# Kernel tuning notes

Hardware: AMD Instinct MI355X
Metric: run time of the kernel (lower is better)

The kernel has to match this reference:

```python
import jax, jax.numpy as jnp
import numpy as np

DIM = 4096; H = 32; D = 128; EPS = 1e-5
BLOCK = 16
BD = 8; MAXB = 64                    # decode seqs, blocks per decode seq
PB = 2; PSEQ = 1024; TP = PB * PSEQ  # prefill: 2 seqs x 1024 tokens
TOK = TP + BD
NBLOCKS = BD * MAXB + TP // BLOCK    # 640
NEG = -1e30


def setup_inputs() -> dict:
    key = jax.random.key(0)
    ks = jax.random.split(key, 10)
    std = 0.02
    x = jax.random.normal(ks[0], (TOK, DIM), jnp.float32)
    key_heap = jax.random.normal(ks[1], (NBLOCKS, BLOCK, H, D), jnp.float32)
    val_heap = jax.random.normal(ks[2], (NBLOCKS, BLOCK, H, D), jnp.float32)
    # decode seq i owns blocks [i*MAXB, (i+1)*MAXB); context_len includes the new token
    ctx = jax.random.randint(ks[3], (BD,), 256, MAXB * BLOCK + 1).astype(jnp.int32)
    block_table = (jnp.arange(BD)[:, None] * MAXB + jnp.arange(MAXB)[None, :]).astype(jnp.int32)
    prefill_slots = BD * MAXB * BLOCK + jnp.arange(TP)      # prefill fills blocks after decode region
    decode_slots = jnp.arange(BD) * MAXB * BLOCK + (ctx - 1)  # newest-token slot per decode seq
    slot_mapping = jnp.concatenate([prefill_slots, decode_slots]).astype(jnp.int32)
    cu = (jnp.arange(PB + 1) * PSEQ).astype(jnp.int32)
    return dict(
        x=x, key_heap=key_heap, val_heap=val_heap,
        slot_mapping=slot_mapping, decode_block_table=block_table,
        decode_context_lens=ctx, prefill_cu_seqlens=cu,
        num_prefill_tokens=TP, prefill_max_seqlen=PSEQ, decode_max_seq_len=MAXB * BLOCK,
        norm1_w=1.0 + std * jax.random.normal(ks[4], (DIM,), jnp.float32),
        norm2_w=1.0 + std * jax.random.normal(ks[5], (DIM,), jnp.float32),
        w_qkv_w=std * jax.random.normal(ks[6], (3 * H * D, DIM), jnp.float32),
        wo_w=std * jax.random.normal(ks[7], (DIM, H * D), jnp.float32),
        w_gate_up_w=std * jax.random.normal(ks[8], (8 * DIM, DIM), jnp.float32),
        w2_w=std * jax.random.normal(ks[9], (DIM, 4 * DIM), jnp.float32),
    )


def _rmsnorm(x, w):
    return x * jax.lax.rsqrt(jnp.mean(x * x, -1, keepdims=True) + EPS) * w


def _forward(x, key_heap, val_heap, norm1_w, norm2_w, w_qkv_w, wo_w, w_gate_up_w, w2_w,
             slot_mapping, decode_block_table, decode_context_lens, prefill_cu_seqlens,
             num_prefill_tokens):
    T = x.shape[0]
    scale = 1.0 / np.sqrt(D)
    residual = x
    # fused norm1 -> QKV projection
    qkv = (_rmsnorm(x, norm1_w) @ w_qkv_w.T).reshape(T, 3, H, D)
    q, k, v = qkv[:, 0], qkv[:, 1], qkv[:, 2]
    # paged cache write (ops.reshape_and_cache)
    nb, bs = key_heap.shape[0], key_heap.shape[1]
    key_flat = key_heap.reshape(nb * bs, H, D).at[slot_mapping].set(k)
    val_flat = val_heap.reshape(nb * bs, H, D).at[slot_mapping].set(v)
    # prefill: varlen causal self-attention (flash_attn_varlen_func)
    Tp = num_prefill_tokens
    pos = jnp.arange(Tp)
    seg = jnp.searchsorted(prefill_cu_seqlens, pos, side='right') - 1
    mask = (seg[:, None] == seg[None, :]) & (pos[:, None] >= pos[None, :])  # [Tp,Tp]
    s = jnp.einsum('ihd,jhd->hij', q[:Tp], k[:Tp]) * scale
    attn_p = jnp.einsum('hij,jhd->ihd',
                        jax.nn.softmax(jnp.where(mask[None], s, NEG), -1), v[:Tp])
    # decode: paged attention over cached KV (ops.paged_attention_v2)
    kd = key_flat.reshape(nb, bs, H, D)[decode_block_table].reshape(BD, -1, H, D)
    vd = val_flat.reshape(nb, bs, H, D)[decode_block_table].reshape(BD, -1, H, D)
    L = kd.shape[1]
    sd = jnp.einsum('bhd,blhd->bhl', q[Tp:], kd) * scale
    dmask = jnp.arange(L)[None, :] < decode_context_lens[:, None]
    attn_d = jnp.einsum('bhl,blhd->bhd',
                        jax.nn.softmax(jnp.where(dmask[:, None, :], sd, NEG), -1), vd)
    attn = jnp.concatenate([attn_p.reshape(Tp, H * D), attn_d.reshape(BD, H * D)], 0)
    # MLP: wo + residual, norm2, SwiGLU, down-proj, residual
    h = attn @ wo_w.T + residual
    residual = h
    gu = _rmsnorm(h, norm2_w) @ w_gate_up_w.T
    g, u = jnp.split(gu, 2, -1)
    return (jax.nn.silu(g) * u) @ w2_w.T + residual


def reference(x, key_heap, val_heap, slot_mapping, decode_block_table, decode_context_lens,
              prefill_cu_seqlens, num_prefill_tokens, prefill_max_seqlen, decode_max_seq_len,
              norm1_w, norm2_w, w_qkv_w, wo_w, w_gate_up_w, w2_w):
    del prefill_max_seqlen, decode_max_seq_len  # kernel scheduling hints only
    return _forward(x, key_heap, val_heap, norm1_w, norm2_w, w_qkv_w, wo_w, w_gate_up_w, w2_w,
                    slot_mapping, decode_block_table, decode_context_lens, prefill_cu_seqlens,
                    num_prefill_tokens)
```

## Files before the change

kernel.cpp:

```cpp
#include <hip/hip_runtime.h>
#include <hip/hip_bf16.h>
#include <stdint.h>

#define DIMC   4096
#define HC     32
#define DC     128
#define TPC    2048
#define TOKC   2056
#define BDC    8
#define MAXBC  64
#define PSEQC  1024
#define QKVN   12288
#define FFNC   16384
#define PSCALE 0.08838834764831843f

typedef __attribute__((ext_vector_type(8))) short short8;
typedef __attribute__((ext_vector_type(4))) float f32x4;
typedef __attribute__((ext_vector_type(4))) unsigned short u16x4;
typedef __attribute__((ext_vector_type(8))) unsigned short u16x8;

__device__ inline unsigned short f2bf(float f) {
  union { float f; unsigned u; } v; v.f = f;
  unsigned r = v.u + 0x7FFFu + ((v.u >> 16) & 1u);
  return (unsigned short)(r >> 16);
}
__device__ inline float bf2f(unsigned short u) {
  union { unsigned u; float f; } v; v.u = ((unsigned)u) << 16;
  return v.f;
}
__device__ inline f32x4 mfma16(short8 a, short8 b, f32x4 c) {
  return __builtin_amdgcn_mfma_f32_16x16x32_bf16(a, b, c, 0, 0, 0);
}
__device__ inline void gload16(const void* g, void* l) {
  __builtin_amdgcn_global_load_lds(
      (const __attribute__((address_space(1))) void*)g,
      (__attribute__((address_space(3))) void*)l, 16, 0, 0);
}

__global__ __launch_bounds__(256) void cvt_w(
    const float* __restrict__ in, unsigned short* __restrict__ out, long n8)
{
  long i = (long)blockIdx.x * 256 + threadIdx.x;
  const long stride = (long)gridDim.x * 256;
  for (; i < n8; i += stride) {
    f32x4 a = ((const f32x4*)in)[2 * i];
    f32x4 b = ((const f32x4*)in)[2 * i + 1];
    u16x8 o;
#pragma unroll
    for (int j = 0; j < 4; ++j) { o[j] = f2bf(a[j]); o[j + 4] = f2bf(b[j]); }
    ((u16x8*)out)[i] = o;
  }
}

__global__ __launch_bounds__(256) void rmsnorm_k(
    const float* __restrict__ x, const float* __restrict__ w,
    unsigned short* __restrict__ out)
{
  const int row = blockIdx.x;
  const int tid = threadIdx.x;
  const f32x4* xr = (const f32x4*)(x + (size_t)row * DIMC);
  f32x4 v[4];
  float ss = 0.f;
#pragma unroll
  for (int i = 0; i < 4; ++i) {
    v[i] = xr[i * 256 + tid];
    ss += v[i][0]*v[i][0] + v[i][1]*v[i][1] + v[i][2]*v[i][2] + v[i][3]*v[i][3];
  }
  for (int off = 32; off; off >>= 1) ss += __shfl_xor(ss, off);
  __shared__ float sred[4];
  if ((tid & 63) == 0) sred[tid >> 6] = ss;
  __syncthreads();
  const float rms = rsqrtf((sred[0]+sred[1]+sred[2]+sred[3]) * (1.f/DIMC) + 1e-5f);
  const f32x4* wr = (const f32x4*)w;
#pragma unroll
  for (int i = 0; i < 4; ++i) {
    f32x4 wv = wr[i * 256 + tid];
    u16x4 o;
#pragma unroll
    for (int j = 0; j < 4; ++j) o[j] = f2bf(v[i][j] * rms * wv[j]);
    *(u16x4*)(out + (size_t)row * DIMC + (size_t)(i * 256 + tid) * 4) = o;
  }
}

template<int MODE>
__global__ __launch_bounds__(512, 2) void gemm8p(
    const unsigned short* __restrict__ A, const unsigned short* __restrict__ Bh,
    float* __restrict__ Cf, unsigned short* __restrict__ Cb,
    const float* __restrict__ Res, int M, int N, int K)
{
  __shared__ char ldsc[131072];
  const int tid = threadIdx.x;
  const int lane = tid & 63, wid = tid >> 6;
  const int wr = wid >> 2, wc = wid & 3;
  const int lhi = lane >> 4, llo = lane & 15;

  const int nM = (M + 255) >> 8;
  const int nwg = gridDim.x, orig = blockIdx.x;
  const int qq = nwg >> 3, rr = nwg & 7;
  const int xcd = orig & 7, lid = orig >> 3;
  const int wgid = (xcd < rr ? xcd*(qq+1) : rr*(qq+1) + (xcd-rr)*qq) + lid;
  const int bm = (wgid % nM) << 8;
  const int bn = (wgid / nM) << 8;

  const unsigned short* src[2][2][2];
#pragma unroll
  for (int i = 0; i < 2; ++i) {
    int s = i * 512 + tid;
    int row = s >> 3;
    int chunk = (s & 7) ^ (row & 7);
#pragma unroll
    for (int h = 0; h < 2; ++h) {
      int ga = bm + h * 128 + row; ga = ga < M ? ga : M - 1;
      src[0][h][i] = A  + (size_t)ga * K + chunk * 8;
      src[1][h][i] = Bh + (size_t)(bn + h * 128 + row) * K + chunk * 8;
    }
  }
  const int NT = K >> 6;

#define STG(U, OP, H) do { \
    int bb_ = (((U) & 1) << 16) + ((OP) << 15) + ((H) << 14) + (wid << 10); \
    gload16(src[OP][H][0] + ((size_t)(U) << 6), ldsc + bb_); \
    gload16(src[OP][H][1] + ((size_t)(U) << 6), ldsc + bb_ + 8192); \
  } while (0)

#define LDA(PB, HA) do { _Pragma("unroll") for (int m_ = 0; m_ < 4; ++m_) { \
    int row_ = wr*64 + m_*16 + llo; \
    int rb_ = (PB) + ((HA) << 14) + row_*128; int sx_ = (row_ & 7) << 4; \
    ar[m_][0] = *(const short8*)(ldsc + rb_ + ((lhi*16) ^ sx_)); \
    ar[m_][1] = *(const short8*)(ldsc + rb_ + ((64 + lhi*16) ^ sx_)); } } while (0)

#define LDB(PB, HB, DST) do { _Pragma("unroll") for (int n_ = 0; n_ < 2; ++n_) { \
    int row_ = wc*32 + n_*16 + llo; \
    int rb_ = (PB) + 32768 + ((HB) << 14) + row_*128; int sx_ = (row_ & 7) << 4; \
    DST[n_][0] = *(const short8*)(ldsc + rb_ + ((lhi*16) ^ sx_)); \
    DST[n_][1] = *(const short8*)(ldsc + rb_ + ((64 + lhi*16) ^ sx_)); } } while (0)

#define MM(QA, QB, B_) do { __builtin_amdgcn_s_setprio(1); \
    _Pragma("unroll") for (int m_ = 0; m_ < 4; ++m_) \
    _Pragma("unroll") for (int n_ = 0; n_ < 2; ++n_) { \
      acc[QA][QB][m_][n_] = mfma16(ar[m_][0], B_[n_][0], acc[QA][QB][m_][n_]); \
      acc[QA][QB][m_][n_] = mfma16(ar[m_][1], B_[n_][1], acc[QA][QB][m_][n_]); } \
    __builtin_amdgcn_s_setprio(0); } while (0)

#define WAITL do { asm volatile("s_waitcnt lgkmcnt(0)" ::: "memory"); \
    __builtin_amdgcn_sched_barrier(0); } while (0)
#define BAR __builtin_amdgcn_s_barrier()

  f32x4 acc[2][2][4][2] = {};
  short8 ar[4][2], b0[2][2], b1[2][2];

  STG(0, 0, 0); STG(0, 0, 1); STG(0, 1, 0); STG(0, 1, 1);
  STG(1, 0, 0); STG(1, 1, 0); STG(1, 1, 1);
  asm volatile("s_waitcnt vmcnt(6)" ::: "memory");
  BAR;

  for (int t = 0; t < NT; ++t) {
    const int pb = (t & 1) << 16;
    LDA(pb, 0); LDB(pb, 0, b0);
    if (t + 1 < NT) STG(t + 1, 0, 1);
    BAR; WAITL;
    MM(0, 0, b0);
    BAR;
    LDB(pb, 1, b1);
    if (t + 2 < NT) STG(t + 2, 0, 0);
    BAR; WAITL;
    MM(0, 1, b1);
    BAR;
    LDA(pb, 1);
    if (t + 2 < NT) STG(t + 2, 1, 0);
    BAR; WAITL;
    MM(1, 1, b1);
    BAR;
    if (t + 2 < NT) {
      STG(t + 2, 1, 1);
      asm volatile("s_waitcnt vmcnt(6)" ::: "memory");
    } else {
      asm volatile("s_waitcnt vmcnt(0)" ::: "memory");
    }
    BAR;
    __builtin_amdgcn_sched_barrier(0);
    MM(1, 0, b0);
    BAR;
  }

#pragma unroll
  for (int qa = 0; qa < 2; ++qa)
#pragma unroll
  for (int m_ = 0; m_ < 4; ++m_)
#pragma unroll
  for (int j = 0; j < 4; ++j) {
    int row = bm + qa*128 + wr*64 + m_*16 + lhi*4 + j;
    if (row < M) {
#pragma unroll
      for (int qb = 0; qb < 2; ++qb)
#pragma unroll
      for (int n_ = 0; n_ < 2; ++n_) {
        int col = bn + qb*128 + wc*32 + n_*16 + llo;
        float v = acc[qa][qb][m_][n_][j];
        if (MODE == 1) { v += Res[(size_t)row*N + col]; Cf[(size_t)row*N + col] = v; }
        else Cb[(size_t)row*N + col] = f2bf(v);
      }
    }
  }
#undef STG
#undef LDA
#undef LDB
#undef MM
#undef WAITL
#undef BAR
}

template<int MODE, int BF16B>
__global__ __launch_bounds__(256) void gemm_bt(
    const unsigned short* __restrict__ A, const float* __restrict__ Bf,
    const unsigned short* __restrict__ Bh,
    float* __restrict__ Cf, unsigned short* __restrict__ Cb,
    const float* __restrict__ Res, int M, int N, int K)
{
  __shared__ unsigned short la[128 * 64];
  __shared__ unsigned short lb[128 * 64];
  const int tid = threadIdx.x;
  const int lane = tid & 63, wid = tid >> 6;
  const int wr = wid >> 1, wc = wid & 1;
  const int lhi = lane >> 4, llo = lane & 15;

  const int nM = (M + 127) >> 7;
  const int nwg = gridDim.x;
  const int orig = blockIdx.x;
  const int qq = nwg >> 3, rr = nwg & 7;
  const int xcd = orig & 7, lid = orig >> 3;
  const int wgid = (xcd < rr ? xcd * (qq + 1) : rr * (qq + 1) + (xcd - rr) * qq) + lid;
  const int bm = (wgid % nM) * 128;
  const int bn = (wgid / nM) * 128;

  const unsigned short* aSrc[4];
  const unsigned short* bSrcH[4];
  char* aDst[4];
  char* bDst[4];
#pragma unroll
  for (int p = 0; p < 4; ++p) {
    int slot = p * 256 + tid;
    int row = slot >> 3;
    int chunk = (slot & 7) ^ (row & 7);
    int gr = bm + row; gr = gr < M ? gr : M - 1;
    aSrc[p] = A + (size_t)gr * K + chunk * 8;
    aDst[p] = (char*)la + p * 4096 + wid * 1024;
    if (BF16B) {
      bSrcH[p] = Bh + (size_t)(bn + row) * K + chunk * 8;
      bDst[p] = (char*)lb + p * 4096 + wid * 1024;
    }
  }

  f32x4 acc[4][4] = {};

  for (int k0 = 0; k0 < K; k0 += 64) {
#pragma unroll
    for (int p = 0; p < 4; ++p) gload16(aSrc[p] + k0, aDst[p]);
    if (BF16B) {
#pragma unroll
      for (int p = 0; p < 4; ++p) gload16(bSrcH[p] + k0, bDst[p]);
    } else {
#pragma unroll
      for (int p = 0; p < 4; ++p) {
        int idx = p * 256 + tid;
        int row = idx >> 3, c8 = (idx & 7) << 3;
        const float* srcf = Bf + (size_t)(bn + row) * K + k0 + c8;
        f32x4 v0 = *(const f32x4*)srcf;
        f32x4 v1 = *(const f32x4*)(srcf + 4);
        short8 bv;
#pragma unroll
        for (int i = 0; i < 4; ++i) { bv[i] = (short)f2bf(v0[i]); bv[i+4] = (short)f2bf(v1[i]); }
        int byt = (row << 7) + (c8 << 1);
        byt ^= (row & 7) << 4;
        *(short8*)((char*)lb + byt) = bv;
      }
    }
    __syncthreads();
#pragma unroll
    for (int kk = 0; kk < 64; kk += 32) {
      short8 af[4], bfr[4];
#pragma unroll
      for (int m = 0; m < 4; ++m) {
        int row = wr * 64 + m * 16 + llo;
        int byt = (row << 7) + ((kk + lhi * 8) << 1);
        byt ^= (row & 7) << 4;
        af[m] = *(const short8*)((const char*)la + byt);
      }
#pragma unroll
      for (int n = 0; n < 4; ++n) {
        int row = wc * 64 + n * 16 + llo;
        int byt = (row << 7) + ((kk + lhi * 8) << 1);
        byt ^= (row & 7) << 4;
        bfr[n] = *(const short8*)((const char*)lb + byt);
      }
#pragma unroll
      for (int m = 0; m < 4; ++m)
#pragma unroll
        for (int n = 0; n < 4; ++n)
          acc[m][n] = mfma16(af[m], bfr[n], acc[m][n]);
    }
    __syncthreads();
  }

#pragma unroll
  for (int m = 0; m < 4; ++m) {
#pragma unroll
    for (int j = 0; j < 4; ++j) {
      int row = bm + wr * 64 + m * 16 + lhi * 4 + j;
      if (row < M) {
#pragma unroll
        for (int n = 0; n < 4; ++n) {
          int col = bn + wc * 64 + n * 16 + llo;
          float v = acc[m][n][j];
          if (MODE == 1) {
            v += Res[(size_t)row * N + col];
            Cf[(size_t)row * N + col] = v;
          } else {
            Cb[(size_t)row * N + col] = f2bf(v);
          }
        }
      }
    }
  }
}

__global__ __launch_bounds__(256) void prefill_attn(
    const unsigned short* __restrict__ qkv, unsigned short* __restrict__ attnb)
{
  const int h = blockIdx.x, qt = blockIdx.y, s = blockIdx.z;
  const int seq0 = s * PSEQC;
  const int q0 = qt * 64;
  const int tid = threadIdx.x;
  const int lane = tid & 63, w = tid >> 6;
  const int lhi = lane >> 4, llo = lane & 15;

  __shared__ unsigned short lk[64 * 128];
  __shared__ unsigned short lvt[128 * 72];
  __shared__ unsigned short lp[4][16 * 72];

  short8 qf[4];
  {
    const unsigned short* qrow =
        qkv + (size_t)(seq0 + q0 + w * 16 + llo) * QKVN + h * DC;
#pragma unroll
    for (int kk = 0; kk < 4; ++kk)
      qf[kk] = *(const short8*)(qrow + kk * 32 + lhi * 8);
  }

  float m_r[4], l_r[4];
#pragma unroll
  for (int r = 0; r < 4; ++r) { m_r[r] = -1e30f; l_r[r] = 0.f; }
  f32x4 oacc[8] = {};

  const int ntiles = qt + 1;
  for (int t = 0; t < ntiles; ++t) {
    const int j0 = t * 64;
#pragma unroll
    for (int p = 0; p < 4; ++p) {
      int idx = p * 256 + tid;
      int row = idx >> 4, c8 = (idx & 15) << 3;
      short8 kv = *(const short8*)(qkv + (size_t)(seq0 + j0 + row) * QKVN + DIMC + h * DC + c8);
      *(short8*)(lk + row * 128 + (c8 ^ ((row & 7) << 3))) = kv;
    }
#pragma unroll
    for (int p = 0; p < 4; ++p) {
      int idx = p * 256 + tid;
      int j = idx >> 4, c8 = (idx & 15) << 3;
      short8 vv = *(const short8*)(qkv + (size_t)(seq0 + j0 + j) * QKVN + 2 * DIMC + h * DC + c8);
#pragma unroll
      for (int i = 0; i < 8; ++i) {
        int d = c8 + i;
        int jj = j ^ (((d >> 3) & 7) << 3);
        lvt[d * 72 + jj] = (unsigned short)vv[i];
      }
    }
    __syncthreads();

    f32x4 sfr[4] = {};
#pragma unroll
    for (int n = 0; n < 4; ++n) {
      int row = n * 16 + llo;
#pragma unroll
      for (int kk = 0; kk < 4; ++kk) {
        int col = (kk * 32 + lhi * 8) ^ ((row & 7) << 3);
        short8 kf = *(const short8*)(lk + row * 128 + col);
        sfr[n] = mfma16(qf[kk], kf, sfr[n]);
      }
    }

    const bool diag = (t == ntiles - 1);
    const int qbase = q0 + w * 16 + lhi * 4;
    float pv[4][4];
#pragma unroll
    for (int r = 0; r < 4; ++r) {
      float mx = -1e30f;
#pragma unroll
      for (int n = 0; n < 4; ++n) {
        float sv = sfr[n][r] * PSCALE;
        if (diag && (j0 + n * 16 + llo > qbase + r)) sv = -1e30f;
        pv[n][r] = sv;
        mx = fmaxf(mx, sv);
      }
      for (int off = 8; off; off >>= 1) mx = fmaxf(mx, __shfl_xor(mx, off));
      float mnew = fmaxf(m_r[r], mx);
      float alpha = __expf(m_r[r] - mnew);
      m_r[r] = mnew;
      float rs = 0.f;
#pragma unroll
      for (int n = 0; n < 4; ++n) {
        float p = __expf(pv[n][r] - mnew);
        pv[n][r] = p;
        rs += p;
      }
      for (int off = 8; off; off >>= 1) rs += __shfl_xor(rs, off);
      l_r[r] = l_r[r] * alpha + rs;
#pragma unroll
      for (int f = 0; f < 8; ++f) oacc[f][r] *= alpha;
    }

    unsigned short* lpw = lp[w];
#pragma unroll
    for (int r = 0; r < 4; ++r)
#pragma unroll
      for (int n = 0; n < 4; ++n)
        lpw[(lhi * 4 + r) * 72 + n * 16 + llo] = f2bf(pv[n][r]);

#pragma unroll
    for (int kk = 0; kk < 2; ++kk) {
      short8 pf = *(const short8*)(lpw + llo * 72 + kk * 32 + lhi * 8);
#pragma unroll
      for (int f = 0; f < 8; ++f) {
        int d = f * 16 + llo;
        int jb = kk * 32 + lhi * 8;
        int jj = jb ^ (((d >> 3) & 7) << 3);
        short8 vf = *(const short8*)(lvt + d * 72 + jj);
        oacc[f] = mfma16(pf, vf, oacc[f]);
      }
    }
    __syncthreads();
  }

#pragma unroll
  for (int r = 0; r < 4; ++r) {
    int row = seq0 + q0 + w * 16 + lhi * 4 + r;
    float inv = 1.f / l_r[r];
#pragma unroll
    for (int f = 0; f < 8; ++f)
      attnb[(size_t)row * DIMC + h * DC + f * 16 + llo] = f2bf(oacc[f][r] * inv);
  }
}

__global__ __launch_bounds__(256) void decode_attn(
    const unsigned short* __restrict__ qkv,
    const float* __restrict__ kheap, const float* __restrict__ vheap,
    const int* __restrict__ btab, const int* __restrict__ ctxl,
    unsigned short* __restrict__ attnb)
{
  const int h = blockIdx.x, b = blockIdx.y;
  const int ctx = ctxl[b];
  const int tq = TPC + b;
  const int tid = threadIdx.x;
  __shared__ float sq[DC];
  __shared__ float sp[1024];
  __shared__ float sred[4];
  __shared__ float obuf[DC];

  const unsigned short* qrow = qkv + (size_t)tq * QKVN + h * DC;
  if (tid < DC) sq[tid] = bf2f(qrow[tid]);
  __syncthreads();

  float lmax = -1e30f;
#pragma unroll
  for (int i = 0; i < 4; ++i) {
    int l = i * 256 + tid;
    float sv = -1e30f;
    if (l < ctx) {
      float accd = 0.f;
      if (l == ctx - 1) {
        const unsigned short* kn = qkv + (size_t)tq * QKVN + DIMC + h * DC;
        for (int d = 0; d < DC; ++d) accd += sq[d] * bf2f(kn[d]);
      } else {
        int blk = btab[b * MAXBC + (l >> 4)];
        const float* kp = kheap + (((size_t)blk * 16 + (l & 15)) * HC + h) * DC;
#pragma unroll
        for (int d = 0; d < DC; d += 4) {
          f32x4 kv = *(const f32x4*)(kp + d);
          accd += sq[d] * kv[0] + sq[d+1] * kv[1] + sq[d+2] * kv[2] + sq[d+3] * kv[3];
        }
      }
      sv = accd * PSCALE;
    }
    sp[l] = sv;
    lmax = fmaxf(lmax, sv);
  }
  for (int off = 32; off; off >>= 1) lmax = fmaxf(lmax, __shfl_xor(lmax, off));
  if ((tid & 63) == 0) sred[tid >> 6] = lmax;
  __syncthreads();
  const float m = fmaxf(fmaxf(sred[0], sred[1]), fmaxf(sred[2], sred[3]));
  __syncthreads();

  float lsum = 0.f;
#pragma unroll
  for (int i = 0; i < 4; ++i) {
    int l = i * 256 + tid;
    float p = __expf(sp[l] - m);
    sp[l] = p;
    lsum += p;
  }
  for (int off = 32; off; off >>= 1) lsum += __shfl_xor(lsum, off);
  if ((tid & 63) == 0) sred[tid >> 6] = lsum;
  __syncthreads();
  const float denom = sred[0] + sred[1] + sred[2] + sred[3];

  const int d = tid & 127, half = tid >> 7;
  float o = 0.f;
  for (int l = half; l < ctx; l += 2) {
    float p = sp[l];
    float v;
    if (l == ctx - 1) {
      v = bf2f(qkv[(size_t)tq * QKVN + 2 * DIMC + h * DC + d]);
    } else {
      int blk = btab[b * MAXBC + (l >> 4)];
      v = vheap[(((size_t)blk * 16 + (l & 15)) * HC + h) * DC + d];
    }
    o += p * v;
  }
  if (half) obuf[d] = o;
  __syncthreads();
  if (!half)
    attnb[(size_t)tq * DIMC + h * DC + d] = f2bf((o + obuf[d]) / denom);
}

__global__ __launch_bounds__(256) void silu_mul(
    const unsigned short* __restrict__ gu, unsigned short* __restrict__ act)
{
  size_t chunk = (size_t)blockIdx.x * 256 + threadIdx.x;
  size_t row = chunk >> 11;
  int c = (int)(chunk & 2047) << 3;
  const unsigned short* g = gu + row * (2 * FFNC) + c;
  u16x8 gv = *(const u16x8*)g;
  u16x8 uv = *(const u16x8*)(g + FFNC);
  u16x8 o;
#pragma unroll
  for (int i = 0; i < 8; ++i) {
    float gf = bf2f(gv[i]);
    float uf = bf2f(uv[i]);
    float sf = gf / (1.f + __expf(-gf));
    o[i] = f2bf(sf * uf);
  }
  *(u16x8*)(act + row * FFNC + c) = o;
}

extern "C" void kernel_launch(void* const* d_in, const int* in_sizes, int n_in,
                              void* d_out, int out_size, void* d_ws, size_t ws_size,
                              hipStream_t stream) {
  const float* x     = (const float*)d_in[0];
  const float* kheap = (const float*)d_in[1];
  const float* vheap = (const float*)d_in[2];
  const int*   btab  = (const int*)d_in[4];
  const int*   ctxl  = (const int*)d_in[5];
  const float* n1w   = (const float*)d_in[10];
  const float* n2w   = (const float*)d_in[11];
  const float* wqkv  = (const float*)d_in[12];
  const float* wo    = (const float*)d_in[13];
  const float* wgu   = (const float*)d_in[14];
  const float* w2    = (const float*)d_in[15];
  float* out = (float*)d_out;

  char* ws = (char*)d_ws;
  unsigned short* xn   = (unsigned short*)(ws);
  unsigned short* qkvb = (unsigned short*)(ws + 16842752);
  unsigned short* actb = qkvb;
  unsigned short* attn = (unsigned short*)(ws + 16842752 + 67371008);
  float*          hbuf = (float*)(ws + 16842752 + 67371008 + 16842752);
  unsigned short* gub  = (unsigned short*)(ws + 16842752 + 67371008 + 16842752 + 33685504);

  const size_t wbase = 269484032;
  const bool bw = ws_size >= wbase + 536870912ull;
  unsigned short* wqkv_h = (unsigned short*)(ws + wbase);
  unsigned short* wo_h   = (unsigned short*)(ws + wbase + 100663296);
  unsigned short* wgu_h  = (unsigned short*)(ws + wbase + 100663296 + 33554432);
  unsigned short* w2_h   = (unsigned short*)(ws + wbase + 100663296 + 33554432 + 268435456);

  if (bw) {
    cvt_w<<<2048, 256, 0, stream>>>(wqkv, wqkv_h, (long)QKVN * DIMC / 8);
    cvt_w<<<2048, 256, 0, stream>>>(wo,   wo_h,   (long)DIMC * DIMC / 8);
    cvt_w<<<2048, 256, 0, stream>>>(wgu,  wgu_h,  (long)2 * FFNC * DIMC / 8);
    cvt_w<<<2048, 256, 0, stream>>>(w2,   w2_h,   (long)DIMC * FFNC / 8);
  }

  const int nM8 = 9;
  const int nM4 = 17;

  rmsnorm_k<<<TOKC, 256, 0, stream>>>(x, n1w, xn);
  if (bw) gemm8p<2><<<nM8 * (QKVN/256), 512, 0, stream>>>(xn, wqkv_h, nullptr, qkvb, nullptr, TOKC, QKVN, DIMC);
  else    gemm_bt<2,0><<<nM4 * (QKVN/128), 256, 0, stream>>>(xn, wqkv, nullptr, nullptr, qkvb, nullptr, TOKC, QKVN, DIMC);
  prefill_attn<<<dim3(HC, PSEQC / 64, 2), 256, 0, stream>>>(qkvb, attn);
  decode_attn<<<dim3(HC, BDC), 256, 0, stream>>>(qkvb, kheap, vheap, btab, ctxl, attn);
  if (bw) gemm_bt<1,1><<<nM4 * (DIMC/128), 256, 0, stream>>>(attn, nullptr, wo_h, hbuf, nullptr, x, TOKC, DIMC, DIMC);
  else    gemm_bt<1,0><<<nM4 * (DIMC/128), 256, 0, stream>>>(attn, wo, nullptr, hbuf, nullptr, x, TOKC, DIMC, DIMC);
  rmsnorm_k<<<TOKC, 256, 0, stream>>>(hbuf, n2w, xn);
  if (bw) gemm8p<2><<<nM8 * (2*FFNC/256), 512, 0, stream>>>(xn, wgu_h, nullptr, gub, nullptr, TOKC, 2*FFNC, DIMC);
  else    gemm_bt<2,0><<<nM4 * (2*FFNC/128), 256, 0, stream>>>(xn, wgu, nullptr, nullptr, gub, nullptr, TOKC, 2*FFNC, DIMC);
  silu_mul<<<(TOKC * (FFNC / 8)) / 256, 256, 0, stream>>>(gub, actb);
  if (bw) gemm8p<1><<<nM8 * (DIMC/256), 512, 0, stream>>>(actb, w2_h, out, nullptr, hbuf, TOKC, DIMC, FFNC);
  else    gemm_bt<1,0><<<nM4 * (DIMC/128), 256, 0, stream>>>(actb, w2, nullptr, out, nullptr, hbuf, TOKC, DIMC, FFNC);
}
```

Measured before the change: 2.017 ms.

## Add split-K to down-projection GEMM and restructure gemm8p LDS prefetch pipeline

The down-projection GEMM (K=16384, N=4096) only launched 9x16=144 workgroups, which underfills the GPU. It now splits K four ways, writing fp32 partials that a separate reduction kernel sums together with the residual. The shared gemm8p main loop is also rewritten to double-buffer A/B register fragments, prefetching the next tile's LDS reads before the current MFMAs and using vmcnt-gated barriers in place of lgkmcnt waits. The costs are an extra partial buffer of about 135MB plus a reduction pass, and the split-K path is only taken when the workspace is large enough.

```diff
diff --git a/kernel.cpp b/kernel.cpp
--- a/kernel.cpp
+++ b/kernel.cpp
@@ -82,7 +82,7 @@
   }
 }
 
-template<int MODE>
+template<int MODE, int SK>
 __global__ __launch_bounds__(512, 2) void gemm8p(
     const unsigned short* __restrict__ A, const unsigned short* __restrict__ Bh,
     float* __restrict__ Cf, unsigned short* __restrict__ Cb,
@@ -95,12 +95,19 @@
   const int lhi = lane >> 4, llo = lane & 15;
 
   const int nM = (M + 255) >> 8;
+  const int nN = N >> 8;
   const int nwg = gridDim.x, orig = blockIdx.x;
   const int qq = nwg >> 3, rr = nwg & 7;
   const int xcd = orig & 7, lid = orig >> 3;
   const int wgid = (xcd < rr ? xcd*(qq+1) : rr*(qq+1) + (xcd-rr)*qq) + lid;
-  const int bm = (wgid % nM) << 8;
-  const int bn = (wgid / nM) << 8;
+  const int tiles = nM * nN;
+  const int ks = wgid / tiles;
+  const int tile = wgid % tiles;
+  const int bm = (tile % nM) << 8;
+  const int bn = (tile / nM) << 8;
+  const int kLen = K / SK;
+  const int k0 = ks * kLen;
+  const int NT = kLen >> 6;
 
   const unsigned short* src[2][2][2];
 #pragma unroll
@@ -111,11 +118,10 @@
 #pragma unroll
     for (int h = 0; h < 2; ++h) {
       int ga = bm + h * 128 + row; ga = ga < M ? ga : M - 1;
-      src[0][h][i] = A  + (size_t)ga * K + chunk * 8;
-      src[1][h][i] = Bh + (size_t)(bn + h * 128 + row) * K + chunk * 8;
-    }
-  }
-  const int NT = K >> 6;
+      src[0][h][i] = A  + (size_t)ga * K + k0 + chunk * 8;
+      src[1][h][i] = Bh + (size_t)(bn + h * 128 + row) * K + k0 + chunk * 8;
+    }
+  }
 
 #define STG(U, OP, H) do { \
     int bb_ = (((U) & 1) << 16) + ((OP) << 15) + ((H) << 14) + (wid << 10); \
@@ -123,11 +129,11 @@
     gload16(src[OP][H][1] + ((size_t)(U) << 6), ldsc + bb_ + 8192); \
   } while (0)
 
-#define LDA(PB, HA) do { _Pragma("unroll") for (int m_ = 0; m_ < 4; ++m_) { \
+#define LDA(PB, HA, DST) do { _Pragma("unroll") for (int m_ = 0; m_ < 4; ++m_) { \
     int row_ = wr*64 + m_*16 + llo; \
     int rb_ = (PB) + ((HA) << 14) + row_*128; int sx_ = (row_ & 7) << 4; \
-    ar[m_][0] = *(const short8*)(ldsc + rb_ + ((lhi*16) ^ sx_)); \
-    ar[m_][1] = *(const short8*)(ldsc + rb_ + ((64 + lhi*16) ^ sx_)); } } while (0)
+    DST[m_][0] = *(const short8*)(ldsc + rb_ + ((lhi*16) ^ sx_)); \
+    DST[m_][1] = *(const short8*)(ldsc + rb_ + ((64 + lhi*16) ^ sx_)); } } while (0)
 
 #define LDB(PB, HB, DST) do { _Pragma("unroll") for (int n_ = 0; n_ < 2; ++n_) { \
     int row_ = wc*32 + n_*16 + llo; \
@@ -135,54 +141,47 @@
     DST[n_][0] = *(const short8*)(ldsc + rb_ + ((lhi*16) ^ sx_)); \
     DST[n_][1] = *(const short8*)(ldsc + rb_ + ((64 + lhi*16) ^ sx_)); } } while (0)
 
-#define MM(QA, QB, B_) do { __builtin_amdgcn_s_setprio(1); \
+#define MM(QA, QB, AR_, B_) do { __builtin_amdgcn_s_setprio(1); \
     _Pragma("unroll") for (int m_ = 0; m_ < 4; ++m_) \
     _Pragma("unroll") for (int n_ = 0; n_ < 2; ++n_) { \
-      acc[QA][QB][m_][n_] = mfma16(ar[m_][0], B_[n_][0], acc[QA][QB][m_][n_]); \
-      acc[QA][QB][m_][n_] = mfma16(ar[m_][1], B_[n_][1], acc[QA][QB][m_][n_]); } \
+      acc[QA][QB][m_][n_] = mfma16(AR_[m_][0], B_[n_][0], acc[QA][QB][m_][n_]); \
+      acc[QA][QB][m_][n_] = mfma16(AR_[m_][1], B_[n_][1], acc[QA][QB][m_][n_]); } \
     __builtin_amdgcn_s_setprio(0); } while (0)
 
-#define WAITL do { asm volatile("s_waitcnt lgkmcnt(0)" ::: "memory"); \
-    __builtin_amdgcn_sched_barrier(0); } while (0)
-#define BAR __builtin_amdgcn_s_barrier()
+#define FEN __builtin_amdgcn_sched_barrier(0)
+#define VMB(N) do { FEN; asm volatile("s_waitcnt vmcnt(" #N ")" ::: "memory"); \
+    __builtin_amdgcn_s_barrier(); FEN; } while (0)
 
   f32x4 acc[2][2][4][2] = {};
-  short8 ar[4][2], b0[2][2], b1[2][2];
-
-  STG(0, 0, 0); STG(0, 0, 1); STG(0, 1, 0); STG(0, 1, 1);
+  short8 arA[4][2], arB[4][2], b1[2][2], b0a[2][2], b0b[2][2];
+
+  STG(0, 0, 0); STG(0, 1, 0); STG(0, 1, 1); STG(0, 0, 1);
   STG(1, 0, 0); STG(1, 1, 0); STG(1, 1, 1);
-  asm volatile("s_waitcnt vmcnt(6)" ::: "memory");
-  BAR;
-
-  for (int t = 0; t < NT; ++t) {
-    const int pb = (t & 1) << 16;
-    LDA(pb, 0); LDB(pb, 0, b0);
-    if (t + 1 < NT) STG(t + 1, 0, 1);
-    BAR; WAITL;
-    MM(0, 0, b0);
-    BAR;
-    LDB(pb, 1, b1);
-    if (t + 2 < NT) STG(t + 2, 0, 0);
-    BAR; WAITL;
-    MM(0, 1, b1);
-    BAR;
-    LDA(pb, 1);
-    if (t + 2 < NT) STG(t + 2, 1, 0);
-    BAR; WAITL;
-    MM(1, 1, b1);
-    BAR;
-    if (t + 2 < NT) {
-      STG(t + 2, 1, 1);
-      asm volatile("s_waitcnt vmcnt(6)" ::: "memory");
-    } else {
-      asm volatile("s_waitcnt vmcnt(0)" ::: "memory");
-    }
-    BAR;
-    __builtin_amdgcn_sched_barrier(0);
-    MM(1, 0, b0);
-    BAR;
-  }
-
+  VMB(8);
+  LDA(0, 0, arA); LDB(0, 0, b0a);
+
+#define TILE(T, CUR, NXT, V0, V1, V2, V3, S1, S2, L2) do { \
+    const int pbc_ = ((T) & 1) << 16, pbn_ = (((T)+1) & 1) << 16; \
+    LDB(pbc_, 1, b1);        STG((T)+1, 0, 1);               MM(0, 0, arA, CUR); VMB(V0); \
+    LDA(pbc_, 1, arB);       if (S1) STG((T)+2, 0, 0);       MM(0, 1, arA, b1);  VMB(V1); \
+    if (L2) LDA(pbn_, 0, arA); if (S2) STG((T)+2, 1, 0);     MM(1, 1, arB, b1);  VMB(V2); \
+    if (L2) LDB(pbn_, 0, NXT); if (S2) STG((T)+2, 1, 1);     MM(1, 0, arB, CUR); VMB(V3); \
+  } while (0)
+
+  for (int t = 0; t < NT - 2; t += 2) {
+    TILE(t,     b0a, b0b, 8, 8, 8, 8, 1, 1, 1);
+    TILE(t + 1, b0b, b0a, 8, 8, 8, 8, 1, 1, 1);
+  }
+  TILE(NT - 2, b0a, b0b, 8, 6, 4, 2, 0, 0, 1);
+  {
+    const int pbc_ = ((NT - 1) & 1) << 16;
+    LDB(pbc_, 1, b1);   MM(0, 0, arA, b0b); VMB(0);
+    LDA(pbc_, 1, arB);  MM(0, 1, arA, b1);
+    MM(1, 1, arB, b1);
+    MM(1, 0, arB, b0b);
+  }
+
+  float* Pf = (MODE == 3) ? (Cf + (size_t)ks * M * N) : Cf;
 #pragma unroll
   for (int qa = 0; qa < 2; ++qa)
 #pragma unroll
@@ -197,7 +196,8 @@
       for (int n_ = 0; n_ < 2; ++n_) {
         int col = bn + qb*128 + wc*32 + n_*16 + llo;
         float v = acc[qa][qb][m_][n_][j];
-        if (MODE == 1) { v += Res[(size_t)row*N + col]; Cf[(size_t)row*N + col] = v; }
+        if (MODE == 1) { v += Res[(size_t)row*N + col]; Pf[(size_t)row*N + col] = v; }
+        else if (MODE == 3) { Pf[(size_t)row*N + col] = v; }
         else Cb[(size_t)row*N + col] = f2bf(v);
       }
     }
@@ -206,8 +206,21 @@
 #undef LDA
 #undef LDB
 #undef MM
-#undef WAITL
-#undef BAR
+#undef FEN
+#undef VMB
+#undef TILE
+}
+
+__global__ __launch_bounds__(256) void redk(
+    const float* __restrict__ p, const float* __restrict__ res,
+    float* __restrict__ out, long n4)
+{
+  long i = (long)blockIdx.x * 256 + threadIdx.x;
+  if (i >= n4) return;
+  const f32x4* p4 = (const f32x4*)p;
+  f32x4 v = p4[i] + p4[i + n4] + p4[i + 2*n4] + p4[i + 3*n4]
+          + ((const f32x4*)res)[i];
+  ((f32x4*)out)[i] = v;
 }
 
 template<int MODE, int BF16B>
@@ -581,6 +594,9 @@
   unsigned short* wo_h   = (unsigned short*)(ws + wbase + 100663296);
   unsigned short* wgu_h  = (unsigned short*)(ws + wbase + 100663296 + 33554432);
   unsigned short* w2_h   = (unsigned short*)(ws + wbase + 100663296 + 33554432 + 268435456);
+  const size_t pko = wbase + 536870912ull;
+  const bool sk4 = bw && (ws_size >= pko + 134742016ull);
+  float* pbuf = (float*)(ws + pko);
 
   if (bw) {
     cvt_w<<<2048, 256, 0, stream>>>(wqkv, wqkv_h, (long)QKVN * DIMC / 8);
@@ -593,16 +609,22 @@
   const int nM4 = 17;
 
   rmsnorm_k<<<TOKC, 256, 0, stream>>>(x, n1w, xn);
-  if (bw) gemm8p<2><<<nM8 * (QKVN/256), 512, 0, stream>>>(xn, wqkv_h, nullptr, qkvb, nullptr, TOKC, QKVN, DIMC);
+  if (bw) gemm8p<2,1><<<nM8 * (QKVN/256), 512, 0, stream>>>(xn, wqkv_h, nullptr, qkvb, nullptr, TOKC, QKVN, DIMC);
   else    gemm_bt<2,0><<<nM4 * (QKVN/128), 256, 0, stream>>>(xn, wqkv, nullptr, nullptr, qkvb, nullptr, TOKC, QKVN, DIMC);
   prefill_attn<<<dim3(HC, PSEQC / 64, 2), 256, 0, stream>>>(qkvb, attn);
   decode_attn<<<dim3(HC, BDC), 256, 0, stream>>>(qkvb, kheap, vheap, btab, ctxl, attn);
   if (bw) gemm_bt<1,1><<<nM4 * (DIMC/128), 256, 0, stream>>>(attn, nullptr, wo_h, hbuf, nullptr, x, TOKC, DIMC, DIMC);
   else    gemm_bt<1,0><<<nM4 * (DIMC/128), 256, 0, stream>>>(attn, wo, nullptr, hbuf, nullptr, x, TOKC, DIMC, DIMC);
   rmsnorm_k<<<TOKC, 256, 0, stream>>>(hbuf, n2w, xn);
-  if (bw) gemm8p<2><<<nM8 * (2*FFNC/256), 512, 0, stream>>>(xn, wgu_h, nullptr, gub, nullptr, TOKC, 2*FFNC, DIMC);
+  if (bw) gemm8p<2,1><<<nM8 * (2*FFNC/256), 512, 0, stream>>>(xn, wgu_h, nullptr, gub, nullptr, TOKC, 2*FFNC, DIMC);
   else    gemm_bt<2,0><<<nM4 * (2*FFNC/128), 256, 0, stream>>>(xn, wgu, nullptr, nullptr, gub, nullptr, TOKC, 2*FFNC, DIMC);
   silu_mul<<<(TOKC * (FFNC / 8)) / 256, 256, 0, stream>>>(gub, actb);
-  if (bw) gemm8p<1><<<nM8 * (DIMC/256), 512, 0, stream>>>(actb, w2_h, out, nullptr, hbuf, TOKC, DIMC, FFNC);
-  else    gemm_bt<1,0><<<nM4 * (DIMC/128), 256, 0, stream>>>(actb, w2, nullptr, out, nullptr, hbuf, TOKC, DIMC, FFNC);
-}
+  if (sk4) {
+    gemm8p<3,4><<<nM8 * (DIMC/256) * 4, 512, 0, stream>>>(actb, w2_h, pbuf, nullptr, nullptr, TOKC, DIMC, FFNC);
+    redk<<<(TOKC * DIMC / 4 + 255) / 256, 256, 0, stream>>>(pbuf, hbuf, out, (long)TOKC * DIMC / 4);
+  } else if (bw) {
+    gemm8p<1,1><<<nM8 * (DIMC/256), 512, 0, stream>>>(actb, w2_h, out, nullptr, hbuf, TOKC, DIMC, FFNC);
+  } else {
+    gemm_bt<1,0><<<nM4 * (DIMC/128), 256, 0, stream>>>(actb, w2, nullptr, out, nullptr, hbuf, TOKC, DIMC, FFNC);
+  }
+}
```

After: 6.330 ms. 3.14x slower.
